# Kernel optimization log

Measured on AMD Instinct MI355X. Metric: run time of the kernel, lower is better.

## Reference

```python
import jax, jax.numpy as jnp
import numpy as np

NGRAM = 16
SUB = 512  # bytes per sub-block


def byte2image(block, ngram=NGRAM):
    """block: (B, L) int -> (B, 1, ngram*8, L-ngram) float32 in [-1, 1]."""
    B, L = block.shape
    blk = block.astype(jnp.int32)
    # nxt[:, i] = blk[:, i+1], last column zero
    nxt = jnp.concatenate([blk[:, 1:], jnp.zeros((B, 1), jnp.int32)], axis=1)
    # 8 bit-shifted views of the byte stream
    shifts = jnp.stack(
        [((blk << s) & 255) + ((nxt >> (8 - s)) & 255) for s in range(8)],
        axis=1,
    )  # (B, 8, L)
    flat = shifts.reshape(B, -1)  # (B, 8*L)
    parts = [flat] + [jnp.roll(flat, -i, axis=1) for i in range(1, ngram)]
    stacked = jnp.concatenate(parts, axis=1).reshape(B, ngram * 8, L)
    result = stacked[:, :, :-ngram].astype(jnp.float32)
    result = (result / 255.0 - 0.5) / 0.5
    return result[:, None]  # (B, 1, ngram*8, L-ngram)


def byte2image_4k(block, ngram=NGRAM):
    """block: (B, 4096) -> (B, 8, ngram*8, 512-ngram)."""
    return jnp.concatenate(
        [byte2image(block[:, i * SUB:(i + 1) * SUB], ngram) for i in range(8)],
        axis=1,
    )


def setup_inputs() -> dict:
    key = jax.random.key(0)
    kx, kw = jax.random.split(key)
    x = jax.random.randint(kx, (256, 4096), 0, 256, dtype=jnp.int64)
    W = jax.random.normal(kw, (496, 64), dtype=jnp.float32) * 0.02
    return {"x": x, "W": W}


def reference(x, W):
    # ByteFormerWrapper.forward with block_size=4096: byte2image_4k then the
    # (opaque) model; model stood in by a linear head over the image width.
    img = byte2image_4k(x)                      # (B, 8, 128, 496)
    out = jnp.einsum('bchw,wo->bcho', img, W)   # (B, 8, 128, 64)
    return out
```

## Files before the change

### kernel.cpp

```cpp
#include <hip/hip_runtime.h>

typedef unsigned short u16;
typedef unsigned int u32;
typedef _Float16 half8 __attribute__((ext_vector_type(8)));
typedef __attribute__((ext_vector_type(4))) float floatx4;

#define LSTRIDE 72
#define TILE (128 * LSTRIDE)

__global__ __launch_bounds__(256, 4) void byteformer_fused(
    const int* __restrict__ x, const float* __restrict__ Wm,
    float* __restrict__ out) {
  __shared__ __align__(16) u16 arena[2 * TILE];
  __shared__ float part[256];
  __shared__ float csumsh[64];
  u16* As = arena;
  u16* Bs = arena + TILE;

  const int t = threadIdx.x;
  const int mtile = blockIdx.x;
  const int y = blockIdx.y;

  const int wave = t >> 6, lane = t & 63;
  const int wm = wave >> 1, wn = wave & 1;
  const int quad = lane >> 4, l16 = lane & 15;

  const int sA_sub = t >> 4;
  const int sA_kg  = (t >> 1) & 7;
  const int sA_qh  = t & 1;
  const long xrow = ((long)mtile * 16 + sA_sub) * 512;

  floatx4 acc[4][4];
  #pragma unroll
  for (int mt = 0; mt < 4; ++mt)
    #pragma unroll
    for (int nt = 0; nt < 4; ++nt)
      acc[mt][nt] = floatx4{0.f, 0.f, 0.f, 0.f};

  float csum_local = 0.0f;

  int4 ca, cb; int cc;
  float fv[17];

  auto xload = [&](int kc) {
    const int base = kc * 64 + sA_kg * 8;
    ca = *(const int4*)&x[xrow + base];
    cb = *(const int4*)&x[xrow + base + 4];
    cc = (base + 8 < 512) ? x[xrow + base + 8] : 0;
  };

  auto wload = [&](int kc) {
    const int cbase = kc * 64 + 16 * wave - 2 * y - 1;
    #pragma unroll
    for (int j = 0; j < 17; ++j) {
      const int c = cbase + j;
      fv[j] = (c >= 0 && c < 496) ? Wm[c * 64 + lane] : 0.0f;
    }
  };

  auto astage = [&]() {
    const u32 c0 = (u32)ca.x, c1 = (u32)ca.y, c2 = (u32)ca.z, c3 = (u32)ca.w;
    const u32 c4 = (u32)cb.x, c5 = (u32)cb.y, c6 = (u32)cb.z, c7 = (u32)cb.w;
    const u32 c8 = (u32)cc;
    const u32 P0 = ((c0 << 8) | c1) | (((c1 << 8) | c2) << 16);
    const u32 P1 = ((c2 << 8) | c3) | (((c3 << 8) | c4) << 16);
    const u32 P2 = ((c4 << 8) | c5) | (((c5 << 8) | c6) << 16);
    const u32 P3 = ((c6 << 8) | c7) | (((c7 << 8) | c8) << 16);
    u16* arow = &As[(sA_sub * 8 + sA_qh * 4) * LSTRIDE + sA_kg * 8];
    #pragma unroll
    for (int qi = 0; qi < 4; ++qi) {
      const int sh = 8 - (sA_qh * 4 + qi);
      int4 d;
      d.x = (int)(((P0 >> sh) & 0x00FF00FFu) | 0x64006400u);
      d.y = (int)(((P1 >> sh) & 0x00FF00FFu) | 0x64006400u);
      d.z = (int)(((P2 >> sh) & 0x00FF00FFu) | 0x64006400u);
      d.w = (int)(((P3 >> sh) & 0x00FF00FFu) | 0x64006400u);
      *(int4*)(arow + qi * LSTRIDE) = d;
    }
  };

  auto bstage = [&]() {
    #pragma unroll
    for (int j = 1; j <= 16; ++j) csum_local += fv[j];
    u32 hp[9];
    #pragma unroll
    for (int i = 0; i < 8; ++i) {
      u32 h0 = __builtin_bit_cast(unsigned short, (_Float16)fv[2 * i]);
      u32 h1 = __builtin_bit_cast(unsigned short, (_Float16)fv[2 * i + 1]);
      hp[i] = h0 | (h1 << 16);
    }
    hp[8] = (u32)__builtin_bit_cast(unsigned short, (_Float16)fv[16]);
    #pragma unroll
    for (int g = 0; g < 2; ++g) {
      const int mgrp = 2 * wave + g;
      int4 d1;
      d1.x = (int)hp[4 * g + 0];
      d1.y = (int)hp[4 * g + 1];
      d1.z = (int)hp[4 * g + 2];
      d1.w = (int)hp[4 * g + 3];
      *(int4*)&Bs[(64 + lane) * LSTRIDE + mgrp * 8] = d1;
      int4 d0;
      d0.x = (int)((hp[4 * g + 0] >> 16) | (hp[4 * g + 1] << 16));
      d0.y = (int)((hp[4 * g + 1] >> 16) | (hp[4 * g + 2] << 16));
      d0.z = (int)((hp[4 * g + 2] >> 16) | (hp[4 * g + 3] << 16));
      d0.w = (int)((hp[4 * g + 3] >> 16) | (hp[4 * g + 4] << 16));
      *(int4*)&Bs[lane * LSTRIDE + mgrp * 8] = d0;
    }
  };

  auto compute_ks = [&](int ks) {
    const int koff = ks * 32 + quad * 8;
    half8 bf[4];
    #pragma unroll
    for (int nt = 0; nt < 4; ++nt)
      bf[nt] = *(const half8*)&Bs[(wn * 64 + nt * 16 + l16) * LSTRIDE + koff];
    #pragma unroll
    for (int mt = 0; mt < 4; ++mt) {
      half8 af = *(const half8*)&As[(wm * 64 + mt * 16 + l16) * LSTRIDE + koff];
      #pragma unroll
      for (int nt = 0; nt < 4; ++nt)
        acc[mt][nt] = __builtin_amdgcn_mfma_f32_16x16x32_f16(
            af, bf[nt], acc[mt][nt], 0, 0, 0);
    }
  };

  xload(0); wload(0);
  astage(); bstage();
  __syncthreads();

  for (int kc = 0; kc < 8; ++kc) {
    compute_ks(0);
    if (kc < 7) {
      __builtin_amdgcn_sched_barrier(0x38F);
      xload(kc + 1);
      wload(kc + 1);
    }
    compute_ks(1);
    __syncthreads();
    if (kc < 7) {
      astage();
      bstage();
      __syncthreads();
    }
  }

  const float S = 2.0f / 255.0f;
  const float K1 = 1024.0f * S + 1.0f;
  part[t] = csum_local;
  __syncthreads();
  if (t < 64)
    csumsh[t] = K1 * (part[t] + part[t + 64] + part[t + 128] + part[t + 192]);
  __syncthreads();

  float cs[4];
  #pragma unroll
  for (int nt = 0; nt < 4; ++nt) cs[nt] = csumsh[nt * 16 + l16];

  float* ep = (float*)arena;
  #pragma unroll
  for (int h = 0; h < 2; ++h) {
    if (wm == h) {
      #pragma unroll
      for (int mt = 0; mt < 4; ++mt)
        #pragma unroll
        for (int i = 0; i < 4; ++i) {
          const int mr = mt * 16 + quad * 4 + i;
          const int rowbase = (mr >> 3) * 1040 + wn * 512 + (mr & 7) * 64 + l16;
          #pragma unroll
          for (int nt = 0; nt < 4; ++nt)
            ep[rowbase + nt * 16] = __builtin_fmaf(S, acc[mt][nt][i], -cs[nt]);
        }
    }
    __syncthreads();
    const long outb =
        ((long)mtile * 16 + (long)h * 8) * 8192 + (long)y * 1024;
    #pragma unroll
    for (int k2 = 0; k2 < 8; ++k2) {
      const float4 v =
          *(const float4*)((const char*)ep + k2 * 4160 + wave * 1024 + lane * 16);
      *(float4*)&out[outb + (long)k2 * 8192 + wave * 256 + lane * 4] = v;
    }
    if (h == 0) __syncthreads();
  }
}

extern "C" void kernel_launch(void* const* d_in, const int* in_sizes, int n_in,
                              void* d_out, int out_size, void* d_ws, size_t ws_size,
                              hipStream_t stream) {
  const int* x = (const int*)d_in[0];
  const float* Wm = (const float*)d_in[1];
  float* out = (float*)d_out;
  byteformer_fused<<<dim3(128, 8), dim3(256), 0, stream>>>(x, Wm, out);
}
```

Measured before the change: 105.9 us.

## Process two M-tiles per block to reuse staged W tile across MFMAs

Each block now handles two 16-row byte sub-blocks with separate A tiles and accumulators while sharing one staged B (weight) tile. The grid halves, which cuts the redundant per-block W loading, conversion and staging per output. The cost is double the accumulator registers, more LDS, lower occupancy (launch bounds 2), and fewer blocks to fill the GPU. The explicit sched_barrier is removed and prefetch loads are now issued before the first compute step.

```diff
diff --git a/kernel.cpp b/kernel.cpp
--- a/kernel.cpp
+++ b/kernel.cpp
@@ -8,17 +8,18 @@
 #define LSTRIDE 72
 #define TILE (128 * LSTRIDE)
 
-__global__ __launch_bounds__(256, 4) void byteformer_fused(
+__global__ __launch_bounds__(256, 2) void byteformer_fused(
     const int* __restrict__ x, const float* __restrict__ Wm,
     float* __restrict__ out) {
-  __shared__ __align__(16) u16 arena[2 * TILE];
+  __shared__ __align__(16) u16 arena[3 * TILE];
   __shared__ float part[256];
   __shared__ float csumsh[64];
-  u16* As = arena;
-  u16* Bs = arena + TILE;
+  u16* As0 = arena;
+  u16* As1 = arena + TILE;
+  u16* Bs  = arena + 2 * TILE;
 
   const int t = threadIdx.x;
-  const int mtile = blockIdx.x;
+  const int bx = blockIdx.x;
   const int y = blockIdx.y;
 
   const int wave = t >> 6, lane = t & 63;
@@ -28,25 +29,32 @@
   const int sA_sub = t >> 4;
   const int sA_kg  = (t >> 1) & 7;
   const int sA_qh  = t & 1;
-  const long xrow = ((long)mtile * 16 + sA_sub) * 512;
-
-  floatx4 acc[4][4];
+  const long xrow0 = ((long)bx * 32 + sA_sub) * 512;
+  const long xrow1 = xrow0 + 16 * 512;
+
+  floatx4 acc0[4][4], acc1[4][4];
   #pragma unroll
   for (int mt = 0; mt < 4; ++mt)
     #pragma unroll
-    for (int nt = 0; nt < 4; ++nt)
-      acc[mt][nt] = floatx4{0.f, 0.f, 0.f, 0.f};
+    for (int nt = 0; nt < 4; ++nt) {
+      acc0[mt][nt] = floatx4{0.f, 0.f, 0.f, 0.f};
+      acc1[mt][nt] = floatx4{0.f, 0.f, 0.f, 0.f};
+    }
 
   float csum_local = 0.0f;
 
-  int4 ca, cb; int cc;
+  int4 ca0, cb0, ca1, cb1; int cc0, cc1;
   float fv[17];
 
   auto xload = [&](int kc) {
     const int base = kc * 64 + sA_kg * 8;
-    ca = *(const int4*)&x[xrow + base];
-    cb = *(const int4*)&x[xrow + base + 4];
-    cc = (base + 8 < 512) ? x[xrow + base + 8] : 0;
+    ca0 = *(const int4*)&x[xrow0 + base];
+    cb0 = *(const int4*)&x[xrow0 + base + 4];
+    ca1 = *(const int4*)&x[xrow1 + base];
+    cb1 = *(const int4*)&x[xrow1 + base + 4];
+    const bool in = (base + 8 < 512);
+    cc0 = in ? x[xrow0 + base + 8] : 0;
+    cc1 = in ? x[xrow1 + base + 8] : 0;
   };
 
   auto wload = [&](int kc) {
@@ -58,10 +66,10 @@
     }
   };
 
-  auto astage = [&]() {
-    const u32 c0 = (u32)ca.x, c1 = (u32)ca.y, c2 = (u32)ca.z, c3 = (u32)ca.w;
-    const u32 c4 = (u32)cb.x, c5 = (u32)cb.y, c6 = (u32)cb.z, c7 = (u32)cb.w;
-    const u32 c8 = (u32)cc;
+  auto astage = [&](u16* As, const int4& a, const int4& b, int c8v) {
+    const u32 c0 = (u32)a.x, c1 = (u32)a.y, c2 = (u32)a.z, c3 = (u32)a.w;
+    const u32 c4 = (u32)b.x, c5 = (u32)b.y, c6 = (u32)b.z, c7 = (u32)b.w;
+    const u32 c8 = (u32)c8v;
     const u32 P0 = ((c0 << 8) | c1) | (((c1 << 8) | c2) << 16);
     const u32 P1 = ((c2 << 8) | c3) | (((c3 << 8) | c4) << 16);
     const u32 P2 = ((c4 << 8) | c5) | (((c5 << 8) | c6) << 16);
@@ -116,29 +124,33 @@
       bf[nt] = *(const half8*)&Bs[(wn * 64 + nt * 16 + l16) * LSTRIDE + koff];
     #pragma unroll
     for (int mt = 0; mt < 4; ++mt) {
-      half8 af = *(const half8*)&As[(wm * 64 + mt * 16 + l16) * LSTRIDE + koff];
+      const int ar = (wm * 64 + mt * 16 + l16) * LSTRIDE + koff;
+      half8 af0 = *(const half8*)&As0[ar];
+      half8 af1 = *(const half8*)&As1[ar];
       #pragma unroll
-      for (int nt = 0; nt < 4; ++nt)
-        acc[mt][nt] = __builtin_amdgcn_mfma_f32_16x16x32_f16(
-            af, bf[nt], acc[mt][nt], 0, 0, 0);
+      for (int nt = 0; nt < 4; ++nt) {
+        acc0[mt][nt] = __builtin_amdgcn_mfma_f32_16x16x32_f16(
+            af0, bf[nt], acc0[mt][nt], 0, 0, 0);
+        acc1[mt][nt] = __builtin_amdgcn_mfma_f32_16x16x32_f16(
+            af1, bf[nt], acc1[mt][nt], 0, 0, 0);
+      }
     }
   };
 
   xload(0); wload(0);
-  astage(); bstage();
+  astage(As0, ca0, cb0, cc0);
+  astage(As1, ca1, cb1, cc1);
+  bstage();
   __syncthreads();
 
   for (int kc = 0; kc < 8; ++kc) {
+    if (kc < 7) { xload(kc + 1); wload(kc + 1); }
     compute_ks(0);
-    if (kc < 7) {
-      __builtin_amdgcn_sched_barrier(0x38F);
-      xload(kc + 1);
-      wload(kc + 1);
-    }
     compute_ks(1);
     __syncthreads();
     if (kc < 7) {
-      astage();
+      astage(As0, ca0, cb0, cc0);
+      astage(As1, ca1, cb1, cc1);
       bstage();
       __syncthreads();
     }
@@ -157,30 +169,35 @@
   for (int nt = 0; nt < 4; ++nt) cs[nt] = csumsh[nt * 16 + l16];
 
   float* ep = (float*)arena;
+  auto epi_fill = [&](const floatx4 (&A)[4][4]) {
+    #pragma unroll
+    for (int mt = 0; mt < 4; ++mt)
+      #pragma unroll
+      for (int i = 0; i < 4; ++i) {
+        const int mr = mt * 16 + quad * 4 + i;
+        const int rowbase = (mr >> 3) * 1040 + wn * 512 + (mr & 7) * 64 + l16;
+        #pragma unroll
+        for (int nt = 0; nt < 4; ++nt)
+          ep[rowbase + nt * 16] = __builtin_fmaf(S, A[mt][nt][i], -cs[nt]);
+      }
+  };
+
   #pragma unroll
-  for (int h = 0; h < 2; ++h) {
-    if (wm == h) {
-      #pragma unroll
-      for (int mt = 0; mt < 4; ++mt)
-        #pragma unroll
-        for (int i = 0; i < 4; ++i) {
-          const int mr = mt * 16 + quad * 4 + i;
-          const int rowbase = (mr >> 3) * 1040 + wn * 512 + (mr & 7) * 64 + l16;
-          #pragma unroll
-          for (int nt = 0; nt < 4; ++nt)
-            ep[rowbase + nt * 16] = __builtin_fmaf(S, acc[mt][nt][i], -cs[nt]);
-        }
+  for (int h = 0; h < 4; ++h) {
+    const int mi = h >> 1, hh = h & 1;
+    if (wm == hh) {
+      if (mi == 0) epi_fill(acc0); else epi_fill(acc1);
     }
     __syncthreads();
     const long outb =
-        ((long)mtile * 16 + (long)h * 8) * 8192 + (long)y * 1024;
+        ((long)(2 * bx + mi) * 16 + (long)hh * 8) * 8192 + (long)y * 1024;
     #pragma unroll
     for (int k2 = 0; k2 < 8; ++k2) {
       const float4 v =
           *(const float4*)((const char*)ep + k2 * 4160 + wave * 1024 + lane * 16);
       *(float4*)&out[outb + (long)k2 * 8192 + wave * 256 + lane * 4] = v;
     }
-    if (h == 0) __syncthreads();
+    if (h < 3) __syncthreads();
   }
 }
 
@@ -190,5 +207,5 @@
   const int* x = (const int*)d_in[0];
   const float* Wm = (const float*)d_in[1];
   float* out = (float*)d_out;
-  byteformer_fused<<<dim3(128, 8), dim3(256), 0, stream>>>(x, Wm, out);
+  byteformer_fused<<<dim3(64, 8), dim3(256), 0, stream>>>(x, Wm, out);
 }
```

Result: faster. 102.2 us (-3.4%).
